# Kernel optimization log

Hardware: AMD Instinct MI355X
Metric: run time of the kernel (lower is better)

## Reference

```python
import jax, jax.numpy as jnp
import numpy as np

MAX_NUM_CAPS = 10
NEG = -1e9

def _layernorm(x, g, b):
    m = x.mean(-1, keepdims=True)
    v = x.var(-1, keepdims=True)
    return (x - m) / jnp.sqrt(v + 1e-5) * g + b

def _gatv2(x, Wl, Wr, att, bias, adj):
    # x: [B,M,F]; Wl/Wr: [F,H*C]; att: [H,C]; adj: [B,M,M] bool, adj[b,i,j] = edge i->j
    B, M, F = x.shape
    H, C = att.shape
    xl = jnp.einsum('bmf,fhc->bmhc', x, Wl.reshape(F, H, C))  # source transform
    xr = jnp.einsum('bmf,fhc->bmhc', x, Wr.reshape(F, H, C))  # target transform
    # GATv2 score: att . leaky_relu(xl[i] + xr[j]) for edge (src=i, dst=j)
    z = jax.nn.leaky_relu(xl[:, :, None, :, :] + xr[:, None, :, :, :], 0.2)  # [B,i,j,H,C]
    e = jnp.einsum('bijhc,hc->bijh', z, att)
    e = jnp.where(adj[..., None], e, NEG)
    alpha = jax.nn.softmax(e, axis=1)  # softmax over incoming sources i per target j
    out = jnp.einsum('bijh,bihc->bjhc', alpha, xl)  # aggregate at targets
    return out.reshape(B, M, H * C) + bias

def setup_inputs() -> dict:
    key = jax.random.key(0)
    ks = jax.random.split(key, 16)
    B, N, T = 128, 16, 48
    Fm, H, C3 = 128, 4, 64
    s = 0.05
    inp = {
        'team_obs': jax.random.normal(ks[0], (B, N, 14), jnp.float32),
        'target_obs': jax.random.normal(ks[1], (B, T, 15), jnp.float32),
        'team_mask': jax.random.normal(ks[2], (B, 2, N), jnp.float32),
        'local_target_mask': jnp.ones((B, T + 1), jnp.float32),
        'W_emb': jax.random.normal(ks[3], (16, Fm), jnp.float32) * s,
        'b_emb': jnp.zeros((Fm,), jnp.float32),
        'Wl1': jax.random.normal(ks[4], (Fm, Fm), jnp.float32) * s,
        'Wr1': jax.random.normal(ks[5], (Fm, Fm), jnp.float32) * s,
        'att1': jax.random.normal(ks[6], (H, Fm // H), jnp.float32) * s,
        'b1': jnp.zeros((Fm,), jnp.float32),
        'Wl2': jax.random.normal(ks[7], (Fm, Fm), jnp.float32) * s,
        'Wr2': jax.random.normal(ks[8], (Fm, Fm), jnp.float32) * s,
        'att2': jax.random.normal(ks[9], (H, Fm // H), jnp.float32) * s,
        'b2': jnp.zeros((Fm,), jnp.float32),
        'Wl3': jax.random.normal(ks[10], (Fm, C3), jnp.float32) * s,
        'Wr3': jax.random.normal(ks[11], (Fm, C3), jnp.float32) * s,
        'att3': jax.random.normal(ks[12], (1, C3), jnp.float32) * s,
        'b3': jnp.zeros((C3,), jnp.float32),
        'ln1_g': jnp.ones((Fm,), jnp.float32),
        'ln1_b': jnp.zeros((Fm,), jnp.float32),
        'ln2_g': jnp.ones((Fm,), jnp.float32),
        'ln2_b': jnp.zeros((Fm,), jnp.float32),
    }
    return inp

def reference(team_obs, target_obs, team_mask, local_target_mask,
              W_emb, b_emb, Wl1, Wr1, att1, b1, Wl2, Wr2, att2, b2,
              Wl3, Wr3, att3, b3, ln1_g, ln1_b, ln2_g, ln2_b):
    B, N, _ = team_obs.shape
    team = jnp.concatenate([team_obs, jnp.zeros((B, N, 2), team_obs.dtype)], axis=2)
    tgt = target_obs[:, :, :-1]
    T = tgt.shape[1]
    tgt = jnp.concatenate([tgt[:, :, :2 + MAX_NUM_CAPS],
                           jnp.zeros((B, T, 2), tgt.dtype),
                           tgt[:, :, -2:]], axis=2)
    fin = jnp.concatenate([team, tgt], axis=1)  # [B, M, inp_dim]
    h = fin @ W_emb + b_emb  # [B, M, 128]
    imp_team = team_mask[:, 0] != -1e9          # [B, N]
    imp_tgt = local_target_mask[:, :-1] != 0.0  # [B, T]
    imp = jnp.concatenate([imp_team, imp_tgt], axis=1)  # [B, M]
    M = N + T
    eye = jnp.eye(M, dtype=bool)
    # edges among active nodes minus diagonal; PyG GATv2Conv add_self_loops=True re-adds self edges
    adj = (imp[:, :, None] & imp[:, None, :] & ~eye) | eye  # [B, M, M]
    out = jax.nn.relu(_layernorm(_gatv2(h, Wl1, Wr1, att1, b1, adj), ln1_g, ln1_b))
    out = jax.nn.relu(_layernorm(_gatv2(out, Wl2, Wr2, att2, b2, adj), ln2_g, ln2_b))
    out = _gatv2(out, Wl3, Wr3, att3, b3, adj)
    return out  # [B, M, out_dim]
```

## Files before the change

### kernel.cpp

```cpp
#include <hip/hip_runtime.h>

typedef unsigned short u16;
typedef unsigned int   u32;
typedef _Float16 h2  __attribute__((ext_vector_type(2)));
typedef __fp16   hw2 __attribute__((ext_vector_type(2)));
typedef __fp16   hw8 __attribute__((ext_vector_type(8)));
typedef float    f4  __attribute__((ext_vector_type(4)));

#define XS 136

static __device__ __forceinline__ h2 pk(float a, float b) {
    return __builtin_bit_cast(h2, __builtin_amdgcn_cvt_pkrtz(a, b));
}
static __device__ __forceinline__ float dot2(h2 a, h2 b, float c) {
    return __builtin_amdgcn_fdot2(__builtin_bit_cast(hw2, a),
                                  __builtin_bit_cast(hw2, b), c, false);
}
static __device__ __forceinline__ h2  b2h(u32 v) { return __builtin_bit_cast(h2, v); }
static __device__ __forceinline__ u32 h2u(h2 v)  { return __builtin_bit_cast(u32, v); }
static __device__ __forceinline__ h2  abs2(h2 v) { return b2h(h2u(v) & 0x7fff7fffu); }
static __device__ __forceinline__ u16 f2h(float f) { return __builtin_bit_cast(u16, (_Float16)f); }
static __device__ __forceinline__ float h2f(u16 v) { return (float)__builtin_bit_cast(_Float16, v); }
static __device__ __forceinline__ f4 mfma16(uint4 a, uint4 b, f4 c) {
    return __builtin_amdgcn_mfma_f32_16x16x32_f16(__builtin_bit_cast(hw8, a),
                                                  __builtin_bit_cast(hw8, b), c, 0, 0, 0);
}
static __device__ __forceinline__ h2 shflx32(h2 v) {
    return b2h((u32)__shfl_xor((int)h2u(v), 32));
}

__global__ void pack_weights(const float* __restrict__ Wl1, const float* __restrict__ Wr1,
                             const float* __restrict__ Wl2, const float* __restrict__ Wr2,
                             const float* __restrict__ Wl3, const float* __restrict__ Wr3,
                             u32* __restrict__ wpk)
{
    const int o = blockIdx.x * 256 + threadIdx.x;
    const float* src; u32* dst; int local; int N;
    if      (o < 8192)  { src = Wl1; dst = wpk;         local = o;         N = 128; }
    else if (o < 16384) { src = Wr1; dst = wpk + 8192;  local = o - 8192;  N = 128; }
    else if (o < 24576) { src = Wl2; dst = wpk + 16384; local = o - 16384; N = 128; }
    else if (o < 32768) { src = Wr2; dst = wpk + 24576; local = o - 24576; N = 128; }
    else if (o < 36864) { src = Wl3; dst = wpk + 32768; local = o - 32768; N = 64;  }
    else                { src = Wr3; dst = wpk + 36864; local = o - 36864; N = 64;  }
    const int i2   = local & 3;
    const int lane = (local >> 2) & 63;
    const int frag = local >> 8;
    const int kb   = frag & 3;
    const int nt   = frag >> 2;
    const int k0   = kb*32 + ((lane >> 4) << 3) + i2*2;
    const int n    = nt*16 + (lane & 15);
    dst[local] = h2u(pk(src[k0*N + n], src[(k0+1)*N + n]));
}

static __device__ __forceinline__ void compute_imp(int t, int b,
    const float* __restrict__ team_mask, const float* __restrict__ ltm, float* sImp)
{
    if (t < 64) {
        float im;
        if (t < 16) im = (team_mask[b*32 + t] != -1000000000.0f) ? 1.f : 0.f;
        else        im = (ltm[b*49 + (t-16)] != 0.0f) ? 1.f : 0.f;
        sImp[t] = im;
    }
}

static __device__ __forceinline__ void matmul128(int w, int lane,
    const u32* __restrict__ wpkL, const u32* __restrict__ wpkR,
    const u16* sX, u16* sXl, uint4* sXrP)
{
    const int  mt  = w & 3;
    const bool isR = (w >= 4);
    const u32* wp  = isR ? wpkR : wpkL;
    const int  n15 = lane & 15;
    const int  qd  = lane >> 4;
    uint4 afr[4];
#pragma unroll
    for (int kb = 0; kb < 4; kb++)
        afr[kb] = *(const uint4*)&sX[(mt*16 + n15)*XS + kb*32 + (qd << 3)];
#pragma unroll
    for (int nt = 0; nt < 8; nt++) {
        f4 acc = {0.f, 0.f, 0.f, 0.f};
#pragma unroll
        for (int kb = 0; kb < 4; kb++) {
            uint4 bf = *(const uint4*)&wp[((nt*4 + kb)*64 + lane)*4];
            acc = mfma16(afr[kb], bf, acc);
        }
        const int n  = nt*16 + n15;
        const int mb = mt*16 + (qd << 2);
        if (!isR) {
#pragma unroll
            for (int r = 0; r < 4; r++) sXl[(mb + r)*XS + n] = f2h(acc[r]);
        } else {
            u16* xp = (u16*)sXrP;
#pragma unroll
            for (int r = 0; r < 4; r++)
                xp[(((n >> 3)*64) + mb + r)*8 + (n & 7)] = f2h(acc[r]);
        }
    }
}

static __device__ __forceinline__ void matmul128g(int w, int lane,
    const u32* __restrict__ wpkL, const u32* __restrict__ wpkR,
    const u32* __restrict__ gxRow, u16* sXl, uint4* sXrP)
{
    const int  mt  = w & 3;
    const bool isR = (w >= 4);
    const u32* wp  = isR ? wpkR : wpkL;
    const int  n15 = lane & 15;
    const int  qd  = lane >> 4;
    const int  m   = mt*16 + n15;
    uint4 afr[4];
#pragma unroll
    for (int kb = 0; kb < 4; kb++)
        afr[kb] = *(const uint4*)&gxRow[m*64 + kb*16 + qd*4];
#pragma unroll
    for (int nt = 0; nt < 8; nt++) {
        f4 acc = {0.f, 0.f, 0.f, 0.f};
#pragma unroll
        for (int kb = 0; kb < 4; kb++) {
            uint4 bf = *(const uint4*)&wp[((nt*4 + kb)*64 + lane)*4];
            acc = mfma16(afr[kb], bf, acc);
        }
        const int n  = nt*16 + n15;
        const int mb = mt*16 + (qd << 2);
        if (!isR) {
#pragma unroll
            for (int r = 0; r < 4; r++) sXl[(mb + r)*XS + n] = f2h(acc[r]);
        } else {
            u16* xp = (u16*)sXrP;
#pragma unroll
            for (int r = 0; r < 4; r++)
                xp[(((n >> 3)*64) + mb + r)*8 + (n & 7)] = f2h(acc[r]);
        }
    }
}

static __device__ __forceinline__ void attn_ln(int t, int w, int lane, int b, int jh,
    const float* __restrict__ att, const float* __restrict__ bias,
    const float* __restrict__ lg, const float* __restrict__ lb,
    u16* sX, const u16* sXl, const uint4* sXrP,
    float* sAl, float* sPart, float* sL2, const float* sImp, u32* __restrict__ gxOut)
{
    const int h  = w & 3;
    const int ih = w >> 2;
    const int jj = lane & 31;
    const int is = lane >> 5;
    const int j  = jh*32 + jj;

    h2 a2[16];
#pragma unroll
    for (int q = 0; q < 16; q++) a2[q] = pk(att[h*32 + 2*q], att[h*32 + 2*q + 1]);

    if (w < 4) {
        const uint4* pr = (const uint4*)&sXl[lane*XS + h*32];
        float al = 0.f;
#pragma unroll
        for (int c4 = 0; c4 < 4; c4++) {
            uint4 v = pr[c4];
            al = dot2(b2h(v.x), a2[c4*4+0], al);
            al = dot2(b2h(v.y), a2[c4*4+1], al);
            al = dot2(b2h(v.z), a2[c4*4+2], al);
            al = dot2(b2h(v.w), a2[c4*4+3], al);
        }
        sAl[h*64 + lane] = al;
    }

    h2 xr2[16];
#pragma unroll
    for (int s = 0; s < 4; s++) {
        uint4 v = sXrP[(h*4 + s)*64 + j];
        xr2[s*4+0] = b2h(v.x); xr2[s*4+1] = b2h(v.y);
        xr2[s*4+2] = b2h(v.z); xr2[s*4+3] = b2h(v.w);
    }
    float Ar = 0.f;
#pragma unroll
    for (int q = 0; q < 16; q++) Ar = dot2(a2[q], xr2[q], Ar);
    const float impj = sImp[j];
    __syncthreads();

    float l = 0.f;
    h2 acc2[16];
#pragma unroll
    for (int q = 0; q < 16; q++) acc2[q] = b2h(0u);
    const int i0 = ih*32 + is*16;
#pragma unroll 4
    for (int ii = 0; ii < 16; ii++) {
        int i = i0 + ii;
        const uint4* pl = (const uint4*)&sXl[i*XS + h*32];
        uint4 v0 = pl[0], v1 = pl[1], v2 = pl[2], v3 = pl[3];
        h2 xl2[16];
        xl2[0] = b2h(v0.x); xl2[1] = b2h(v0.y); xl2[2]  = b2h(v0.z); xl2[3]  = b2h(v0.w);
        xl2[4] = b2h(v1.x); xl2[5] = b2h(v1.y); xl2[6]  = b2h(v1.z); xl2[7]  = b2h(v1.w);
        xl2[8] = b2h(v2.x); xl2[9] = b2h(v2.y); xl2[10] = b2h(v2.z); xl2[11] = b2h(v2.w);
        xl2[12]= b2h(v3.x); xl2[13]= b2h(v3.y); xl2[14] = b2h(v3.z); xl2[15] = b2h(v3.w);
        float S0 = 0.f, S1 = 0.f;
#pragma unroll
        for (int q = 0; q < 16; q += 2) {
            h2 t0 = abs2(xl2[q]   + xr2[q]);
            h2 t1 = abs2(xl2[q+1] + xr2[q+1]);
            S0 = dot2(a2[q],   t0, S0);
            S1 = dot2(a2[q+1], t1, S1);
        }
        float e  = 0.6f*(sAl[h*64 + i] + Ar) + 0.4f*(S0 + S1);
        float ad = (i == j) ? 1.f : impj * sImp[i];
        float p  = (ad != 0.f) ? __expf(e) : 0.f;
        l += p;
        h2 p2 = pk(p, p);
#pragma unroll
        for (int q = 0; q < 16; q++) acc2[q] += p2 * xl2[q];
    }

    l += __shfl_xor(l, 32);
#pragma unroll
    for (int q = 0; q < 16; q++) acc2[q] = acc2[q] + shflx32(acc2[q]);

    u32* ov = (u32*)sX;
    if (w >= 4 && lane < 32) {
        uint4* d4 = (uint4*)(ov + (h*32 + jj)*20);
        uint4 o;
        o.x = h2u(acc2[0]);  o.y = h2u(acc2[1]);  o.z = h2u(acc2[2]);  o.w = h2u(acc2[3]);  d4[0] = o;
        o.x = h2u(acc2[4]);  o.y = h2u(acc2[5]);  o.z = h2u(acc2[6]);  o.w = h2u(acc2[7]);  d4[1] = o;
        o.x = h2u(acc2[8]);  o.y = h2u(acc2[9]);  o.z = h2u(acc2[10]); o.w = h2u(acc2[11]); d4[2] = o;
        o.x = h2u(acc2[12]); o.y = h2u(acc2[13]); o.z = h2u(acc2[14]); o.w = h2u(acc2[15]); d4[3] = o;
        sL2[h*32 + jj] = l;
    }
    __syncthreads();

    float yv[32];
    if (w < 4 && lane < 32) {
        const uint4* s4 = (const uint4*)(ov + (h*32 + jj)*20);
        uint4 u0 = s4[0], u1 = s4[1], u2 = s4[2], u3 = s4[3];
        h2 oth[16];
        oth[0] = b2h(u0.x); oth[1] = b2h(u0.y); oth[2]  = b2h(u0.z); oth[3]  = b2h(u0.w);
        oth[4] = b2h(u1.x); oth[5] = b2h(u1.y); oth[6]  = b2h(u1.z); oth[7]  = b2h(u1.w);
        oth[8] = b2h(u2.x); oth[9] = b2h(u2.y); oth[10] = b2h(u2.z); oth[11] = b2h(u2.w);
        oth[12]= b2h(u3.x); oth[13]= b2h(u3.y); oth[14] = b2h(u3.z); oth[15] = b2h(u3.w);
        l += sL2[h*32 + jj];
        const float rl = 1.f / l;
        float s1 = 0.f, s2v = 0.f;
#pragma unroll
        for (int q = 0; q < 16; q++) {
            h2 sum = acc2[q] + oth[q];
            float y0 = fmaf((float)sum[0], rl, bias[h*32 + 2*q]);
            float y1 = fmaf((float)sum[1], rl, bias[h*32 + 2*q + 1]);
            yv[2*q] = y0; yv[2*q+1] = y1;
            s1 += y0 + y1;
            s2v = fmaf(y0, y0, s2v);
            s2v = fmaf(y1, y1, s2v);
        }
        sPart[h*32 + jj]       = s1;
        sPart[128 + h*32 + jj] = s2v;
    }
    __syncthreads();

    if (w < 4 && lane < 32) {
        float su = sPart[jj] + sPart[32 + jj] + sPart[64 + jj] + sPart[96 + jj];
        float sq = sPart[128 + jj] + sPart[160 + jj] + sPart[192 + jj] + sPart[224 + jj];
        const float mean = su * 0.0078125f;
        const float var  = sq * 0.0078125f - mean*mean;
        const float rstd = rsqrtf(var + 1e-5f);
        u32 orow[16];
#pragma unroll
        for (int q = 0; q < 16; q++) {
            int f0 = h*32 + 2*q;
            float v0 = fmaxf(fmaf((yv[2*q]   - mean)*rstd, lg[f0],   lb[f0]),   0.f);
            float v1 = fmaxf(fmaf((yv[2*q+1] - mean)*rstd, lg[f0+1], lb[f0+1]), 0.f);
            orow[q] = h2u(pk(v0, v1));
        }
        uint4* po = (uint4*)(gxOut + (size_t)b*4096 + (size_t)j*64 + h*16);
        po[0] = *(uint4*)&orow[0];
        po[1] = *(uint4*)&orow[4];
        po[2] = *(uint4*)&orow[8];
        po[3] = *(uint4*)&orow[12];
    }
}

__global__ void __launch_bounds__(512, 1) gnn_layer1(
    const float* __restrict__ team_obs, const float* __restrict__ target_obs,
    const float* __restrict__ team_mask, const float* __restrict__ ltm,
    const float* __restrict__ W_emb, const float* __restrict__ b_emb,
    const float* __restrict__ att1, const float* __restrict__ b1,
    const float* __restrict__ ln1_g, const float* __restrict__ ln1_b,
    const u32* __restrict__ wpk, u32* __restrict__ gx1)
{
    __shared__ __align__(16) u16   sX  [64*XS];
    __shared__ __align__(16) u16   sXl [64*XS];
    __shared__ __align__(16) uint4 sXrP[1024];
    __shared__ float sFin[1024];
    __shared__ float sAl [256];
    __shared__ float sPart[256];
    __shared__ float sL2 [128];
    __shared__ float sImp[64];

    const int t    = threadIdx.x;
    const int w    = t >> 6;
    const int lane = t & 63;
    const int b    = blockIdx.x & 127;
    const int jh   = blockIdx.x >> 7;

    compute_imp(t, b, team_mask, ltm, sImp);
    for (int ee = t; ee < 1024; ee += 512) {
        int m = ee >> 4, k = ee & 15;
        float v = 0.f;
        if (m < 16) {
            if (k < 14) v = team_obs[(b*16 + m)*14 + k];
        } else {
            const float* tg = target_obs + (size_t)(b*48 + (m-16))*15;
            if      (k < 12)  v = tg[k];
            else if (k == 14) v = tg[12];
            else if (k == 15) v = tg[13];
        }
        sFin[m*16 + k] = v;
    }
    __syncthreads();

    {
        const int f = t & 127;
        const int g = t >> 7;
        float wreg[16];
#pragma unroll
        for (int k = 0; k < 16; k++) wreg[k] = W_emb[k*128 + f];
        const float bf = b_emb[f];
#pragma unroll
        for (int mm = 0; mm < 16; mm++) {
            int m = g*16 + mm;
            const float4* pf = (const float4*)&sFin[m*16];
            float4 f0 = pf[0], f1 = pf[1], f2 = pf[2], f3 = pf[3];
            float acc = bf;
            acc = fmaf(f0.x, wreg[0],  acc); acc = fmaf(f0.y, wreg[1],  acc);
            acc = fmaf(f0.z, wreg[2],  acc); acc = fmaf(f0.w, wreg[3],  acc);
            acc = fmaf(f1.x, wreg[4],  acc); acc = fmaf(f1.y, wreg[5],  acc);
            acc = fmaf(f1.z, wreg[6],  acc); acc = fmaf(f1.w, wreg[7],  acc);
            acc = fmaf(f2.x, wreg[8],  acc); acc = fmaf(f2.y, wreg[9],  acc);
            acc = fmaf(f2.z, wreg[10], acc); acc = fmaf(f2.w, wreg[11], acc);
            acc = fmaf(f3.x, wreg[12], acc); acc = fmaf(f3.y, wreg[13], acc);
            acc = fmaf(f3.z, wreg[14], acc); acc = fmaf(f3.w, wreg[15], acc);
            sX[m*XS + f] = f2h(acc);
        }
    }
    __syncthreads();

    matmul128(w, lane, wpk, wpk + 8192, sX, sXl, sXrP);
    __syncthreads();
    attn_ln(t, w, lane, b, jh, att1, b1, ln1_g, ln1_b,
            sX, sXl, sXrP, sAl, sPart, sL2, sImp, gx1);
}

__global__ void __launch_bounds__(512, 1) gnn_layer2(
    const float* __restrict__ team_mask, const float* __restrict__ ltm,
    const float* __restrict__ att2, const float* __restrict__ b2,
    const float* __restrict__ ln2_g, const float* __restrict__ ln2_b,
    const u32* __restrict__ wpk, const u32* __restrict__ gxIn, u32* __restrict__ gxOut)
{
    __shared__ __align__(16) u16   sX  [64*XS];
    __shared__ __align__(16) u16   sXl [64*XS];
    __shared__ __align__(16) uint4 sXrP[1024];
    __shared__ float sAl [256];
    __shared__ float sPart[256];
    __shared__ float sL2 [128];
    __shared__ float sImp[64];

    const int t    = threadIdx.x;
    const int w    = t >> 6;
    const int lane = t & 63;
    const int b    = blockIdx.x & 127;
    const int jh   = blockIdx.x >> 7;

    compute_imp(t, b, team_mask, ltm, sImp);
    matmul128g(w, lane, wpk + 16384, wpk + 24576, gxIn + (size_t)b*4096, sXl, sXrP);
    __syncthreads();
    attn_ln(t, w, lane, b, jh, att2, b2, ln2_g, ln2_b,
            sX, sXl, sXrP, sAl, sPart, sL2, sImp, gxOut);
}

__global__ void __launch_bounds__(512, 1) gnn_layer3(
    const float* __restrict__ team_mask, const float* __restrict__ ltm,
    const float* __restrict__ att3, const float* __restrict__ b3,
    const u32* __restrict__ wpk, const u32* __restrict__ gxIn, float* __restrict__ out)
{
    __shared__ __align__(16) u16   sXl [64*XS];
    __shared__ __align__(16) uint4 sXrP[512];
    __shared__ float sAl [64];
    __shared__ float sPart[512];
    __shared__ float sImp[64];
    __shared__ u16   sE  [64*32];

    const int t    = threadIdx.x;
    const int w    = t >> 6;
    const int lane = t & 63;
    const int b    = blockIdx.x & 127;
    const int jh   = blockIdx.x >> 7;

    compute_imp(t, b, team_mask, ltm, sImp);
    const u32* gxRow = gxIn + (size_t)b*4096;

    {
        const int  mt  = w & 3;
        const bool isR = (w >= 4);
        const u32* wp  = isR ? (wpk + 36864) : (wpk + 32768);
        const int  n15 = lane & 15;
        const int  qd  = lane >> 4;
        const int  m   = mt*16 + n15;
        uint4 afr[4];
#pragma unroll
        for (int kb = 0; kb < 4; kb++)
            afr[kb] = *(const uint4*)&gxRow[m*64 + kb*16 + qd*4];
#pragma unroll
        for (int nt = 0; nt < 4; nt++) {
            f4 acc = {0.f, 0.f, 0.f, 0.f};
#pragma unroll
            for (int kb = 0; kb < 4; kb++) {
                uint4 bf = *(const uint4*)&wp[((nt*4 + kb)*64 + lane)*4];
                acc = mfma16(afr[kb], bf, acc);
            }
            const int n  = nt*16 + n15;
            const int mb = mt*16 + (qd << 2);
            if (!isR) {
#pragma unroll
                for (int r = 0; r < 4; r++) sXl[(mb + r)*XS + n] = f2h(acc[r]);
            } else {
                u16* xp = (u16*)sXrP;
#pragma unroll
                for (int r = 0; r < 4; r++)
                    xp[(((n >> 3)*64) + mb + r)*8 + (n & 7)] = f2h(acc[r]);
            }
        }
    }
    __syncthreads();

    {
        h2 a2l[4];
#pragma unroll
        for (int q = 0; q < 4; q++) a2l[q] = pk(att3[w*8 + 2*q], att3[w*8 + 2*q + 1]);
        uint4 v = *(const uint4*)&sXl[lane*XS + w*8];
        float al = 0.f;
        al = dot2(b2h(v.x), a2l[0], al);
        al = dot2(b2h(v.y), a2l[1], al);
        al = dot2(b2h(v.z), a2l[2], al);
        al = dot2(b2h(v.w), a2l[3], al);
        sPart[w*64 + lane] = al;
    }
    __syncthreads();
    if (t < 64) {
        sAl[t] = ((sPart[t] + sPart[64+t]) + (sPart[128+t] + sPart[192+t]))
               + ((sPart[256+t] + sPart[320+t]) + (sPart[384+t] + sPart[448+t]));
    }
    __syncthreads();

    const int jj = lane & 31;
    const int is = lane >> 5;
    const int j  = jh*32 + jj;

    {
        h2 a3[32], xr3[32];
#pragma unroll
        for (int q = 0; q < 32; q++) a3[q] = pk(att3[2*q], att3[2*q + 1]);
#pragma unroll
        for (int s = 0; s < 8; s++) {
            uint4 v = sXrP[s*64 + j];
            xr3[s*4+0] = b2h(v.x); xr3[s*4+1] = b2h(v.y);
            xr3[s*4+2] = b2h(v.z); xr3[s*4+3] = b2h(v.w);
        }
        float Ar = 0.f;
#pragma unroll
        for (int q = 0; q < 32; q++) Ar = dot2(a3[q], xr3[q], Ar);
        const float impj = sImp[j];
        const int ib = (w*2 + is)*4;
        for (int ii = 0; ii < 4; ii++) {
            int i = ib + ii;
            const uint4* pl = (const uint4*)&sXl[i*XS];
            float S0 = 0.f, S1 = 0.f;
#pragma unroll
            for (int c4 = 0; c4 < 8; c4++) {
                uint4 v = pl[c4];
                S0 = dot2(a3[c4*4+0], abs2(b2h(v.x) + xr3[c4*4+0]), S0);
                S1 = dot2(a3[c4*4+1], abs2(b2h(v.y) + xr3[c4*4+1]), S1);
                S0 = dot2(a3[c4*4+2], abs2(b2h(v.z) + xr3[c4*4+2]), S0);
                S1 = dot2(a3[c4*4+3], abs2(b2h(v.w) + xr3[c4*4+3]), S1);
            }
            float e  = 0.6f*(sAl[i] + Ar) + 0.4f*(S0 + S1);
            float ad = (i == j) ? 1.f : impj * sImp[i];
            e = (ad != 0.f) ? e : -60000.0f;
            sE[i*32 + jj] = f2h(e);
        }
    }
    __syncthreads();

    {
        const int c0 = w*8;
        h2 acc2[4];
#pragma unroll
        for (int q = 0; q < 4; q++) acc2[q] = b2h(0u);
        float l = 0.f;
        for (int k = 0; k < 32; k++) {
            int i = is*32 + k;
            float p = __expf(h2f(sE[i*32 + jj]));
            l += p;
            h2 p2 = pk(p, p);
            uint4 v = *(const uint4*)&sXl[i*XS + c0];
            acc2[0] += p2 * b2h(v.x);
            acc2[1] += p2 * b2h(v.y);
            acc2[2] += p2 * b2h(v.z);
            acc2[3] += p2 * b2h(v.w);
        }
        l += __shfl_xor(l, 32);
#pragma unroll
        for (int q = 0; q < 4; q++) acc2[q] = acc2[q] + shflx32(acc2[q]);
        if (is == 0) {
            const float rl = 1.f / l;
            float o[8];
#pragma unroll
            for (int q = 0; q < 4; q++) {
                o[2*q]   = fmaf((float)acc2[q][0], rl, b3[c0 + 2*q]);
                o[2*q+1] = fmaf((float)acc2[q][1], rl, b3[c0 + 2*q + 1]);
            }
            float4* po = (float4*)(out + (size_t)b*4096 + (size_t)j*64 + c0);
            po[0] = *(const float4*)&o[0];
            po[1] = *(const float4*)&o[4];
        }
    }
}

extern "C" void kernel_launch(void* const* d_in, const int* in_sizes, int n_in,
                              void* d_out, int out_size, void* d_ws, size_t ws_size,
                              hipStream_t stream) {
    (void)in_sizes; (void)n_in; (void)ws_size; (void)out_size;
    const float* team_obs          = (const float*)d_in[0];
    const float* target_obs        = (const float*)d_in[1];
    const float* team_mask         = (const float*)d_in[2];
    const float* local_target_mask = (const float*)d_in[3];
    const float* W_emb             = (const float*)d_in[4];
    const float* b_emb             = (const float*)d_in[5];
    const float* Wl1               = (const float*)d_in[6];
    const float* Wr1               = (const float*)d_in[7];
    const float* att1              = (const float*)d_in[8];
    const float* b1                = (const float*)d_in[9];
    const float* Wl2               = (const float*)d_in[10];
    const float* Wr2               = (const float*)d_in[11];
    const float* att2              = (const float*)d_in[12];
    const float* b2                = (const float*)d_in[13];
    const float* Wl3               = (const float*)d_in[14];
    const float* Wr3               = (const float*)d_in[15];
    const float* att3              = (const float*)d_in[16];
    const float* b3                = (const float*)d_in[17];
    const float* ln1_g             = (const float*)d_in[18];
    const float* ln1_b             = (const float*)d_in[19];
    const float* ln2_g             = (const float*)d_in[20];
    const float* ln2_b             = (const float*)d_in[21];
    float* out = (float*)d_out;

    u32* wpk = (u32*)d_ws;
    u32* gx2 = (u32*)d_ws + 40960;
    u32* gx1 = (u32*)d_out;

    pack_weights<<<dim3(160), dim3(256), 0, stream>>>(Wl1, Wr1, Wl2, Wr2, Wl3, Wr3, wpk);
    gnn_layer1<<<dim3(256), dim3(512), 0, stream>>>(
        team_obs, target_obs, team_mask, local_target_mask, W_emb, b_emb,
        att1, b1, ln1_g, ln1_b, wpk, gx1);
    gnn_layer2<<<dim3(256), dim3(512), 0, stream>>>(
        team_mask, local_target_mask, att2, b2, ln2_g, ln2_b, wpk, gx1, gx2);
    gnn_layer3<<<dim3(256), dim3(512), 0, stream>>>(
        team_mask, local_target_mask, att3, b3, wpk, gx2, out);
}
```

Measured before the change: 138.6 us.

## Fuse three GATv2 layers into one per-graph kernel keeping activations in LDS

Replaces the three per-layer kernels (each launched with 256 blocks splitting targets in halves) with a single kernel of 128 blocks, one per graph, that runs all three layers and keeps intermediate activations in shared memory. This removes two kernel launches and the global round-trips of layer outputs, and drops the cross-lane shuffle reductions because each lane now owns a full target. In exchange, each block now does twice the per-thread attention work and the grid is halved to 128 blocks, which leaves many of the MI355X's compute units idle. Shared-memory use per block also grows.

```diff
diff --git a/kernel.cpp b/kernel.cpp
--- a/kernel.cpp
+++ b/kernel.cpp
@@ -24,9 +24,6 @@
 static __device__ __forceinline__ f4 mfma16(uint4 a, uint4 b, f4 c) {
     return __builtin_amdgcn_mfma_f32_16x16x32_f16(__builtin_bit_cast(hw8, a),
                                                   __builtin_bit_cast(hw8, b), c, 0, 0, 0);
-}
-static __device__ __forceinline__ h2 shflx32(h2 v) {
-    return b2h((u32)__shfl_xor((int)h2u(v), 32));
 }
 
 __global__ void pack_weights(const float* __restrict__ Wl1, const float* __restrict__ Wr1,
@@ -98,53 +95,15 @@
     }
 }
 
-static __device__ __forceinline__ void matmul128g(int w, int lane,
-    const u32* __restrict__ wpkL, const u32* __restrict__ wpkR,
-    const u32* __restrict__ gxRow, u16* sXl, uint4* sXrP)
-{
-    const int  mt  = w & 3;
-    const bool isR = (w >= 4);
-    const u32* wp  = isR ? wpkR : wpkL;
-    const int  n15 = lane & 15;
-    const int  qd  = lane >> 4;
-    const int  m   = mt*16 + n15;
-    uint4 afr[4];
-#pragma unroll
-    for (int kb = 0; kb < 4; kb++)
-        afr[kb] = *(const uint4*)&gxRow[m*64 + kb*16 + qd*4];
-#pragma unroll
-    for (int nt = 0; nt < 8; nt++) {
-        f4 acc = {0.f, 0.f, 0.f, 0.f};
-#pragma unroll
-        for (int kb = 0; kb < 4; kb++) {
-            uint4 bf = *(const uint4*)&wp[((nt*4 + kb)*64 + lane)*4];
-            acc = mfma16(afr[kb], bf, acc);
-        }
-        const int n  = nt*16 + n15;
-        const int mb = mt*16 + (qd << 2);
-        if (!isR) {
-#pragma unroll
-            for (int r = 0; r < 4; r++) sXl[(mb + r)*XS + n] = f2h(acc[r]);
-        } else {
-            u16* xp = (u16*)sXrP;
-#pragma unroll
-            for (int r = 0; r < 4; r++)
-                xp[(((n >> 3)*64) + mb + r)*8 + (n & 7)] = f2h(acc[r]);
-        }
-    }
-}
-
-static __device__ __forceinline__ void attn_ln(int t, int w, int lane, int b, int jh,
+static __device__ __forceinline__ void attn_ln_fused(int w, int lane,
     const float* __restrict__ att, const float* __restrict__ bias,
     const float* __restrict__ lg, const float* __restrict__ lb,
-    u16* sX, const u16* sXl, const uint4* sXrP,
-    float* sAl, float* sPart, float* sL2, const float* sImp, u32* __restrict__ gxOut)
+    u16* sXout, const u16* sXl, const uint4* sXrP,
+    float* sAl, float* sPart, float* sL2, const float* sImp, u32* sOv)
 {
     const int h  = w & 3;
-    const int ih = w >> 2;
-    const int jj = lane & 31;
-    const int is = lane >> 5;
-    const int j  = jh*32 + jj;
+    const int hf = w >> 2;
+    const int j  = lane;
 
     h2 a2[16];
 #pragma unroll
@@ -181,10 +140,10 @@
     h2 acc2[16];
 #pragma unroll
     for (int q = 0; q < 16; q++) acc2[q] = b2h(0u);
-    const int i0 = ih*32 + is*16;
+    const int i0 = hf*32;
 #pragma unroll 4
-    for (int ii = 0; ii < 16; ii++) {
-        int i = i0 + ii;
+    for (int ii = 0; ii < 32; ii++) {
+        const int i = i0 + ii;
         const uint4* pl = (const uint4*)&sXl[i*XS + h*32];
         uint4 v0 = pl[0], v1 = pl[1], v2 = pl[2], v3 = pl[3];
         h2 xl2[16];
@@ -209,32 +168,27 @@
         for (int q = 0; q < 16; q++) acc2[q] += p2 * xl2[q];
     }
 
-    l += __shfl_xor(l, 32);
-#pragma unroll
-    for (int q = 0; q < 16; q++) acc2[q] = acc2[q] + shflx32(acc2[q]);
-
-    u32* ov = (u32*)sX;
-    if (w >= 4 && lane < 32) {
-        uint4* d4 = (uint4*)(ov + (h*32 + jj)*20);
+    if (hf == 1) {
+        uint4* d4 = (uint4*)(sOv + (h*64 + j)*20);
         uint4 o;
         o.x = h2u(acc2[0]);  o.y = h2u(acc2[1]);  o.z = h2u(acc2[2]);  o.w = h2u(acc2[3]);  d4[0] = o;
         o.x = h2u(acc2[4]);  o.y = h2u(acc2[5]);  o.z = h2u(acc2[6]);  o.w = h2u(acc2[7]);  d4[1] = o;
         o.x = h2u(acc2[8]);  o.y = h2u(acc2[9]);  o.z = h2u(acc2[10]); o.w = h2u(acc2[11]); d4[2] = o;
         o.x = h2u(acc2[12]); o.y = h2u(acc2[13]); o.z = h2u(acc2[14]); o.w = h2u(acc2[15]); d4[3] = o;
-        sL2[h*32 + jj] = l;
+        sL2[h*64 + j] = l;
     }
     __syncthreads();
 
     float yv[32];
-    if (w < 4 && lane < 32) {
-        const uint4* s4 = (const uint4*)(ov + (h*32 + jj)*20);
+    if (hf == 0) {
+        const uint4* s4 = (const uint4*)(sOv + (h*64 + j)*20);
         uint4 u0 = s4[0], u1 = s4[1], u2 = s4[2], u3 = s4[3];
         h2 oth[16];
         oth[0] = b2h(u0.x); oth[1] = b2h(u0.y); oth[2]  = b2h(u0.z); oth[3]  = b2h(u0.w);
         oth[4] = b2h(u1.x); oth[5] = b2h(u1.y); oth[6]  = b2h(u1.z); oth[7]  = b2h(u1.w);
         oth[8] = b2h(u2.x); oth[9] = b2h(u2.y); oth[10] = b2h(u2.z); oth[11] = b2h(u2.w);
         oth[12]= b2h(u3.x); oth[13]= b2h(u3.y); oth[14] = b2h(u3.z); oth[15] = b2h(u3.w);
-        l += sL2[h*32 + jj];
+        l += sL2[h*64 + j];
         const float rl = 1.f / l;
         float s1 = 0.f, s2v = 0.f;
 #pragma unroll
@@ -247,14 +201,14 @@
             s2v = fmaf(y0, y0, s2v);
             s2v = fmaf(y1, y1, s2v);
         }
-        sPart[h*32 + jj]       = s1;
-        sPart[128 + h*32 + jj] = s2v;
-    }
-    __syncthreads();
-
-    if (w < 4 && lane < 32) {
-        float su = sPart[jj] + sPart[32 + jj] + sPart[64 + jj] + sPart[96 + jj];
-        float sq = sPart[128 + jj] + sPart[160 + jj] + sPart[192 + jj] + sPart[224 + jj];
+        sPart[h*64 + j]       = s1;
+        sPart[256 + h*64 + j] = s2v;
+    }
+    __syncthreads();
+
+    if (hf == 0) {
+        float su = sPart[j] + sPart[64 + j] + sPart[128 + j] + sPart[192 + j];
+        float sq = sPart[256 + j] + sPart[320 + j] + sPart[384 + j] + sPart[448 + j];
         const float mean = su * 0.0078125f;
         const float var  = sq * 0.0078125f - mean*mean;
         const float rstd = rsqrtf(var + 1e-5f);
@@ -266,7 +220,7 @@
             float v1 = fmaxf(fmaf((yv[2*q+1] - mean)*rstd, lg[f0+1], lb[f0+1]), 0.f);
             orow[q] = h2u(pk(v0, v1));
         }
-        uint4* po = (uint4*)(gxOut + (size_t)b*4096 + (size_t)j*64 + h*16);
+        uint4* po = (uint4*)&sXout[j*XS + h*32];
         po[0] = *(uint4*)&orow[0];
         po[1] = *(uint4*)&orow[4];
         po[2] = *(uint4*)&orow[8];
@@ -274,28 +228,31 @@
     }
 }
 
-__global__ void __launch_bounds__(512, 1) gnn_layer1(
+__global__ void __launch_bounds__(512, 1) gnn_fused(
     const float* __restrict__ team_obs, const float* __restrict__ target_obs,
     const float* __restrict__ team_mask, const float* __restrict__ ltm,
     const float* __restrict__ W_emb, const float* __restrict__ b_emb,
     const float* __restrict__ att1, const float* __restrict__ b1,
     const float* __restrict__ ln1_g, const float* __restrict__ ln1_b,
-    const u32* __restrict__ wpk, u32* __restrict__ gx1)
+    const float* __restrict__ att2, const float* __restrict__ b2,
+    const float* __restrict__ ln2_g, const float* __restrict__ ln2_b,
+    const float* __restrict__ att3, const float* __restrict__ b3,
+    const u32* __restrict__ wpk, float* __restrict__ out)
 {
     __shared__ __align__(16) u16   sX  [64*XS];
     __shared__ __align__(16) u16   sXl [64*XS];
     __shared__ __align__(16) uint4 sXrP[1024];
     __shared__ float sFin[1024];
     __shared__ float sAl [256];
-    __shared__ float sPart[256];
-    __shared__ float sL2 [128];
+    __shared__ float sPart[512];
+    __shared__ float sL2 [256];
     __shared__ float sImp[64];
+    __shared__ __align__(16) u32 sOv[5120];
 
     const int t    = threadIdx.x;
     const int w    = t >> 6;
     const int lane = t & 63;
-    const int b    = blockIdx.x & 127;
-    const int jh   = blockIdx.x >> 7;
+    const int b    = blockIdx.x;
 
     compute_imp(t, b, team_mask, ltm, sImp);
     for (int ee = t; ee < 1024; ee += 512) {
@@ -341,57 +298,15 @@
 
     matmul128(w, lane, wpk, wpk + 8192, sX, sXl, sXrP);
     __syncthreads();
-    attn_ln(t, w, lane, b, jh, att1, b1, ln1_g, ln1_b,
-            sX, sXl, sXrP, sAl, sPart, sL2, sImp, gx1);
-}
-
-__global__ void __launch_bounds__(512, 1) gnn_layer2(
-    const float* __restrict__ team_mask, const float* __restrict__ ltm,
-    const float* __restrict__ att2, const float* __restrict__ b2,
-    const float* __restrict__ ln2_g, const float* __restrict__ ln2_b,
-    const u32* __restrict__ wpk, const u32* __restrict__ gxIn, u32* __restrict__ gxOut)
-{
-    __shared__ __align__(16) u16   sX  [64*XS];
-    __shared__ __align__(16) u16   sXl [64*XS];
-    __shared__ __align__(16) uint4 sXrP[1024];
-    __shared__ float sAl [256];
-    __shared__ float sPart[256];
-    __shared__ float sL2 [128];
-    __shared__ float sImp[64];
-
-    const int t    = threadIdx.x;
-    const int w    = t >> 6;
-    const int lane = t & 63;
-    const int b    = blockIdx.x & 127;
-    const int jh   = blockIdx.x >> 7;
-
-    compute_imp(t, b, team_mask, ltm, sImp);
-    matmul128g(w, lane, wpk + 16384, wpk + 24576, gxIn + (size_t)b*4096, sXl, sXrP);
-    __syncthreads();
-    attn_ln(t, w, lane, b, jh, att2, b2, ln2_g, ln2_b,
-            sX, sXl, sXrP, sAl, sPart, sL2, sImp, gxOut);
-}
-
-__global__ void __launch_bounds__(512, 1) gnn_layer3(
-    const float* __restrict__ team_mask, const float* __restrict__ ltm,
-    const float* __restrict__ att3, const float* __restrict__ b3,
-    const u32* __restrict__ wpk, const u32* __restrict__ gxIn, float* __restrict__ out)
-{
-    __shared__ __align__(16) u16   sXl [64*XS];
-    __shared__ __align__(16) uint4 sXrP[512];
-    __shared__ float sAl [64];
-    __shared__ float sPart[512];
-    __shared__ float sImp[64];
-    __shared__ u16   sE  [64*32];
-
-    const int t    = threadIdx.x;
-    const int w    = t >> 6;
-    const int lane = t & 63;
-    const int b    = blockIdx.x & 127;
-    const int jh   = blockIdx.x >> 7;
-
-    compute_imp(t, b, team_mask, ltm, sImp);
-    const u32* gxRow = gxIn + (size_t)b*4096;
+    attn_ln_fused(w, lane, att1, b1, ln1_g, ln1_b,
+                  sX, sXl, sXrP, sAl, sPart, sL2, sImp, sOv);
+    __syncthreads();
+
+    matmul128(w, lane, wpk + 16384, wpk + 24576, sX, sXl, sXrP);
+    __syncthreads();
+    attn_ln_fused(w, lane, att2, b2, ln2_g, ln2_b,
+                  sX, sXl, sXrP, sAl, sPart, sL2, sImp, sOv);
+    __syncthreads();
 
     {
         const int  mt  = w & 3;
@@ -399,11 +314,10 @@
         const u32* wp  = isR ? (wpk + 36864) : (wpk + 32768);
         const int  n15 = lane & 15;
         const int  qd  = lane >> 4;
-        const int  m   = mt*16 + n15;
         uint4 afr[4];
 #pragma unroll
         for (int kb = 0; kb < 4; kb++)
-            afr[kb] = *(const uint4*)&gxRow[m*64 + kb*16 + qd*4];
+            afr[kb] = *(const uint4*)&sX[(mt*16 + n15)*XS + kb*32 + (qd << 3)];
 #pragma unroll
         for (int nt = 0; nt < 4; nt++) {
             f4 acc = {0.f, 0.f, 0.f, 0.f};
@@ -446,9 +360,7 @@
     }
     __syncthreads();
 
-    const int jj = lane & 31;
-    const int is = lane >> 5;
-    const int j  = jh*32 + jj;
+    u16* sE = (u16*)sOv;
 
     {
         h2 a3[32], xr3[32];
@@ -456,17 +368,17 @@
         for (int q = 0; q < 32; q++) a3[q] = pk(att3[2*q], att3[2*q + 1]);
 #pragma unroll
         for (int s = 0; s < 8; s++) {
-            uint4 v = sXrP[s*64 + j];
+            uint4 v = sXrP[s*64 + lane];
             xr3[s*4+0] = b2h(v.x); xr3[s*4+1] = b2h(v.y);
             xr3[s*4+2] = b2h(v.z); xr3[s*4+3] = b2h(v.w);
         }
         float Ar = 0.f;
 #pragma unroll
         for (int q = 0; q < 32; q++) Ar = dot2(a3[q], xr3[q], Ar);
-        const float impj = sImp[j];
-        const int ib = (w*2 + is)*4;
-        for (int ii = 0; ii < 4; ii++) {
-            int i = ib + ii;
+        const float impj = sImp[lane];
+#pragma unroll
+        for (int ii = 0; ii < 8; ii++) {
+            const int i = w*8 + ii;
             const uint4* pl = (const uint4*)&sXl[i*XS];
             float S0 = 0.f, S1 = 0.f;
 #pragma unroll
@@ -478,9 +390,9 @@
                 S1 = dot2(a3[c4*4+3], abs2(b2h(v.w) + xr3[c4*4+3]), S1);
             }
             float e  = 0.6f*(sAl[i] + Ar) + 0.4f*(S0 + S1);
-            float ad = (i == j) ? 1.f : impj * sImp[i];
+            float ad = (i == lane) ? 1.f : impj * sImp[i];
             e = (ad != 0.f) ? e : -60000.0f;
-            sE[i*32 + jj] = f2h(e);
+            sE[i*64 + lane] = f2h(e);
         }
     }
     __syncthreads();
@@ -491,9 +403,8 @@
 #pragma unroll
         for (int q = 0; q < 4; q++) acc2[q] = b2h(0u);
         float l = 0.f;
-        for (int k = 0; k < 32; k++) {
-            int i = is*32 + k;
-            float p = __expf(h2f(sE[i*32 + jj]));
+        for (int i = 0; i < 64; i++) {
+            float p = __expf(h2f(sE[i*64 + lane]));
             l += p;
             h2 p2 = pk(p, p);
             uint4 v = *(const uint4*)&sXl[i*XS + c0];
@@ -502,21 +413,16 @@
             acc2[2] += p2 * b2h(v.z);
             acc2[3] += p2 * b2h(v.w);
         }
-        l += __shfl_xor(l, 32);
-#pragma unroll
-        for (int q = 0; q < 4; q++) acc2[q] = acc2[q] + shflx32(acc2[q]);
-        if (is == 0) {
-            const float rl = 1.f / l;
-            float o[8];
-#pragma unroll
-            for (int q = 0; q < 4; q++) {
-                o[2*q]   = fmaf((float)acc2[q][0], rl, b3[c0 + 2*q]);
-                o[2*q+1] = fmaf((float)acc2[q][1], rl, b3[c0 + 2*q + 1]);
-            }
-            float4* po = (float4*)(out + (size_t)b*4096 + (size_t)j*64 + c0);
-            po[0] = *(const float4*)&o[0];
-            po[1] = *(const float4*)&o[4];
-        }
+        const float rl = 1.f / l;
+        float o[8];
+#pragma unroll
+        for (int q = 0; q < 4; q++) {
+            o[2*q]   = fmaf((float)acc2[q][0], rl, b3[c0 + 2*q]);
+            o[2*q+1] = fmaf((float)acc2[q][1], rl, b3[c0 + 2*q + 1]);
+        }
+        float4* po = (float4*)(out + (size_t)b*4096 + (size_t)lane*64 + c0);
+        po[0] = *(const float4*)&o[0];
+        po[1] = *(const float4*)&o[4];
     }
 }
 
@@ -549,15 +455,9 @@
     float* out = (float*)d_out;
 
     u32* wpk = (u32*)d_ws;
-    u32* gx2 = (u32*)d_ws + 40960;
-    u32* gx1 = (u32*)d_out;
 
     pack_weights<<<dim3(160), dim3(256), 0, stream>>>(Wl1, Wr1, Wl2, Wr2, Wl3, Wr3, wpk);
-    gnn_layer1<<<dim3(256), dim3(512), 0, stream>>>(
+    gnn_fused<<<dim3(128), dim3(512), 0, stream>>>(
         team_obs, target_obs, team_mask, local_target_mask, W_emb, b_emb,
-        att1, b1, ln1_g, ln1_b, wpk, gx1);
-    gnn_layer2<<<dim3(256), dim3(512), 0, stream>>>(
-        team_mask, local_target_mask, att2, b2, ln2_g, ln2_b, wpk, gx1, gx2);
-    gnn_layer3<<<dim3(256), dim3(512), 0, stream>>>(
-        team_mask, local_target_mask, att3, b3, wpk, gx2, out);
-}
+        att1, b1, ln1_g, ln1_b, att2, b2, ln2_g, ln2_b, att3, b3, wpk, out);
+}
```

New measurement: 146.4 us. 1.06x slower.
